# Kernel tuning notes

Measured on AMD Instinct MI355X. Metric: run time of the kernel, lower is better.

Reference implementation:

```python
import jax, jax.numpy as jnp
import numpy as np

T, B, H, W, CIN = 20, 16, 128, 128, 2
CH, OUT = 64, 10
BETA, THR = 0.9, 1.0


def spike(u):
    # Heaviside fire (surrogate grad only matters in bwd module)
    return (u > 0.0).astype(u.dtype)


def setup_inputs() -> dict:
    key = jax.random.key(0)
    k0, k1, k2 = jax.random.split(key, 3)
    x_seq = jax.random.normal(k0, (T, B, H, W, CIN), jnp.float32)
    w_conv = jax.random.normal(k1, (3, 3, CIN, CH), jnp.float32) * (1.0 / np.sqrt(9 * CIN))
    b_conv = jnp.zeros((CH,), jnp.float32)
    w_head = jax.random.normal(k2, (CH, OUT), jnp.float32) * (1.0 / np.sqrt(CH))
    b_head = jnp.zeros((OUT,), jnp.float32)
    return {"x_seq": x_seq, "w_conv": w_conv, "b_conv": b_conv,
            "w_head": w_head, "b_head": b_head}


def reference(x_seq, w_conv, b_conv, w_head, b_head):
    # temporal frame differences: [T-1, B, H, W, CIN]
    flow = x_seq[1:] - x_seq[:-1]
    t, b, h, w, c = flow.shape
    # conv is carry-independent: batch it over (time*batch) in one call
    u = jax.lax.conv_general_dilated(
        flow.reshape(t * b, h, w, c), w_conv,
        window_strides=(1, 1), padding='SAME',
        dimension_numbers=('NHWC', 'HWIO', 'NHWC')) + b_conv
    u = u.reshape(t, b, h, w, CH)  # [T-1, B, H, W, CH]

    def step(V, u_t):
        # LIF: leaky integrate, fire, soft reset
        V = BETA * V + u_t
        s = spike(V - THR)
        V = V - s * THR
        y = jnp.mean(s, axis=(1, 2)) @ w_head + b_head  # [B, OUT]
        return V, (y, jnp.mean(s))

    V0 = jnp.zeros((b, h, w, CH), u.dtype)
    _, (logits_seq, sr_seq) = jax.lax.scan(step, V0, u)
    readout = jnp.mean(logits_seq, axis=0)  # 'mean' readout
    return readout, logits_seq, jnp.asarray([jnp.mean(sr_seq)])
```

## Files before the change

kernel.cpp:

```cpp
#include <hip/hip_runtime.h>
#include <hip/hip_bf16.h>

#define TT   20
#define TS   19
#define BB   16
#define HH   128
#define WW   128
#define CINN 2
#define CHN  64
#define NOUT 10
#define BETA 0.9f
#define INVB (1.0f / BETA)
#define THRV 1.0f

#define NCHUNK 5
#define NPB    128
#define SR_IDX (BB*NOUT + TS*BB*NOUT)

#define LROW  20

typedef __attribute__((ext_vector_type(8))) short short8;
typedef __attribute__((ext_vector_type(4))) float float4v;
typedef __attribute__((ext_vector_type(4))) int   int4v;

__device__ __forceinline__ unsigned rne16(float f) {
    unsigned u = __float_as_uint(f);
    return (u + 0x7fffu + ((u >> 16) & 1u)) >> 16;
}
__device__ __forceinline__ float b2f(unsigned us) { return __uint_as_float(us << 16); }
__device__ __forceinline__ unsigned rndb(float f) {
    unsigned u = __float_as_uint(f);
    return u + 0x7fffu + ((u >> 16) & 1u);
}
__device__ __forceinline__ void pack2(float d0, float d1, unsigned &hi, unsigned &lo) {
    unsigned r0 = rndb(d0), r1 = rndb(d1);
    hi = __builtin_amdgcn_perm(r1, r0, 0x07060302u);
    float e0 = d0 - __uint_as_float(r0 & 0xffff0000u);
    float e1 = d1 - __uint_as_float(r1 & 0xffff0000u);
    lo = __builtin_amdgcn_perm(rndb(e1), rndb(e0), 0x07060302u);
}

__global__ __launch_bounds__(256, 4) void lif_main(const float* __restrict__ x,
                                                   const float* __restrict__ w_conv,
                                                   const float* __restrict__ b_conv,
                                                   int* __restrict__ ws,
                                                   float* __restrict__ out) {
    __shared__ unsigned lds[4][2][2][4 * LROW];
    __shared__ int lds_cnt[NCHUNK][CHN];

    const float2* xp2 = (const float2*)x;
    const int FRAME2  = BB * HH * WW;

    const int tid  = threadIdx.x;
    const int lane = tid & 63;
    const int wv   = __builtin_amdgcn_readfirstlane(tid >> 6);
    const int bx   = blockIdx.x;
    const int r0   = blockIdx.y << 1;
    const int bz   = blockIdx.z;
    const int q    = lane >> 4;
    const int col  = lane & 15;
    const int x0   = (bx << 6) + (wv << 4);
    const int qsh  = q << 3;

    if (bx == 0 && blockIdx.y == 0 && bz == 0) {
        if (tid < BB * NOUT) out[tid] = 0.f;
        else if (tid == BB * NOUT) out[SR_IDX] = 0.f;
    }

    if (tid < NCHUNK * CHN - 256) ((int*)lds_cnt)[256 + tid] = 0;
    ((int*)lds_cnt)[tid] = 0;
    __syncthreads();

    const int  row0 = lane / 18, dx0 = lane - row0 * 18;
    const int  y0s  = r0 - 1 + row0;
    const int  px0s = x0 - 1 + dx0;
    const bool val0 = ((unsigned)y0s < (unsigned)HH) && ((unsigned)px0s < (unsigned)WW);
    const int  off0 = val0 ? (y0s * WW + px0s) : 0;
    const int  ls0  = row0 * LROW + dx0;

    const bool act1 = (lane < 8);
    const int  y1s  = r0 + 2;
    const int  px1s = x0 - 1 + 10 + lane;
    const bool val1 = act1 && ((unsigned)y1s < (unsigned)HH) && ((unsigned)px1s < (unsigned)WW);
    const int  off1 = val1 ? (y1s * WW + px1s) : 0;
    const int  ls1  = 3 * LROW + 10 + lane;

    const int rq  = (q < 3) ? q : 0;
    const int rdb = rq * LROW + col;

    short8 Bh[4], Bl[4];
#pragma unroll
    for (int cg = 0; cg < 4; ++cg) {
        int hi_i[4] = {0, 0, 0, 0}, lo_i[4] = {0, 0, 0, 0};
        if (q < 3) {
#pragma unroll
            for (int j = 0; j < 6; ++j) {
                float w = w_conv[((q * 3 + (j >> 1)) * 2 + (j & 1)) * CHN + cg * 16 + col];
                unsigned hs = rne16(w);
                unsigned ls = rne16(w - b2f(hs));
                hi_i[j >> 1] |= (int)(hs << (16 * (j & 1)));
                lo_i[j >> 1] |= (int)(ls << (16 * (j & 1)));
            }
        }
        int4v hv = {hi_i[0], hi_i[1], hi_i[2], hi_i[3]};
        int4v lv = {lo_i[0], lo_i[1], lo_i[2], lo_i[3]};
        Bh[cg] = __builtin_bit_cast(short8, hv);
        Bl[cg] = __builtin_bit_cast(short8, lv);
    }

    float nb[4];
#pragma unroll
    for (int cg = 0; cg < 4; ++cg) nb[cg] = -b_conv[cg * 16 + col];

    float4v W0[4], W1[4];
#pragma unroll
    for (int cg = 0; cg < 4; ++cg) {
        W0[cg] = (float4v){0.f, 0.f, 0.f, 0.f};
        W1[cg] = (float4v){0.f, 0.f, 0.f, 0.f};
    }

    float ct = 1.0f;
    float S  = 1.0f;
    int pendA = 0, pendB = 0;
    unsigned cur = 0;

    float2 ra_0 = {0.f, 0.f}, rb_0 = {0.f, 0.f}, rc_0 = {0.f, 0.f};
    float2 ra_1 = {0.f, 0.f}, rb_1 = {0.f, 0.f}, rc_1 = {0.f, 0.f};
    const float2* xb = xp2 + bz * HH * WW;
    if (val0) { rb_0 = xb[off0]; ra_0 = xb[FRAME2 + off0]; rc_0 = xb[2 * FRAME2 + off0]; }
    if (val1) { rb_1 = xb[off1]; ra_1 = xb[FRAME2 + off1]; rc_1 = xb[2 * FRAME2 + off1]; }
    {
        unsigned* hiW = &lds[wv][0][0][0];
        unsigned* loW = &lds[wv][0][1][0];
        {
            float d0 = (ra_0.x - rb_0.x), d1 = (ra_0.y - rb_0.y);
            unsigned hw, lw; pack2(d0, d1, hw, lw);
            hiW[ls0] = hw; loW[ls0] = lw;
        }
        if (act1) {
            float d0 = (ra_1.x - rb_1.x), d1 = (ra_1.y - rb_1.y);
            unsigned hw, lw; pack2(d0, d1, hw, lw);
            hiW[ls1] = hw; loW[ls1] = lw;
        }
        rb_0 = ra_0; ra_0 = rc_0;
        rb_1 = ra_1; ra_1 = rc_1;
        if (val0) rc_0 = xb[3 * FRAME2 + off0];
        if (val1) rc_1 = xb[3 * FRAME2 + off1];
    }
    const float2* xn = xb + 4 * FRAME2;

#define STEP(T_, CURB, NXTB, DPOS, DODEF, DOFLUSH, CK, DOSTAGE, DOPREF) do {    \
    const unsigned* hiR = &lds[wv][CURB][0][0] + rdb;                           \
    const unsigned* loR = &lds[wv][CURB][1][0] + rdb;                           \
    unsigned h0 = hiR[0], h1 = hiR[1], h2 = hiR[2];                             \
    unsigned h3 = hiR[LROW], h4 = hiR[LROW + 1], h5 = hiR[LROW + 2];            \
    unsigned l0 = loR[0], l1 = loR[1], l2 = loR[2];                             \
    unsigned l3 = loR[LROW], l4 = loR[LROW + 1], l5 = loR[LROW + 2];            \
    int cp1_ = 0, sh2_ = 0;                                                     \
    if (DODEF) { cp1_ = pendA + pendB; sh2_ = __shfl_xor(cp1_, 32); }           \
    float ctn = ct * INVB;                                                      \
    if (DOSTAGE) {                                                              \
        unsigned* hiW = &lds[wv][NXTB][0][0];                                   \
        unsigned* loW = &lds[wv][NXTB][1][0];                                   \
        {                                                                       \
            float d0 = (ra_0.x - rb_0.x) * ctn;                                 \
            float d1 = (ra_0.y - rb_0.y) * ctn;                                 \
            unsigned hw, lw; pack2(d0, d1, hw, lw);                             \
            hiW[ls0] = hw; loW[ls0] = lw;                                       \
        }                                                                       \
        if (act1) {                                                             \
            float d0 = (ra_1.x - rb_1.x) * ctn;                                 \
            float d1 = (ra_1.y - rb_1.y) * ctn;                                 \
            unsigned hw, lw; pack2(d0, d1, hw, lw);                             \
            hiW[ls1] = hw; loW[ls1] = lw;                                       \
        }                                                                       \
        rb_0 = ra_0; ra_0 = rc_0;                                               \
        rb_1 = ra_1; ra_1 = rc_1;                                               \
        if (DOPREF) {                                                           \
            if (val0) rc_0 = xn[off0];                                          \
            if (val1) rc_1 = xn[off1];                                          \
            xn += FRAME2;                                                       \
        }                                                                       \
    }                                                                           \
    int4v a0h = {(int)h0, (int)h1, (int)h2, (int)h0};                           \
    int4v a0l = {(int)l0, (int)l1, (int)l2, (int)l0};                           \
    int4v a1h = {(int)h3, (int)h4, (int)h5, (int)h3};                           \
    int4v a1l = {(int)l3, (int)l4, (int)l5, (int)l3};                           \
    short8 A0h = __builtin_bit_cast(short8, a0h);                               \
    short8 A0l = __builtin_bit_cast(short8, a0l);                               \
    short8 A1h = __builtin_bit_cast(short8, a1h);                               \
    short8 A1l = __builtin_bit_cast(short8, a1l);                               \
    __builtin_amdgcn_s_setprio(1);                                              \
    _Pragma("unroll")                                                           \
    for (int cg = 0; cg < 4; ++cg) {                                            \
        W0[cg] = __builtin_amdgcn_mfma_f32_16x16x32_bf16(A0h, Bh[cg], W0[cg], 0, 0, 0); \
        W1[cg] = __builtin_amdgcn_mfma_f32_16x16x32_bf16(A1h, Bh[cg], W1[cg], 0, 0, 0); \
    }                                                                           \
    _Pragma("unroll")                                                           \
    for (int cg = 0; cg < 4; ++cg) {                                            \
        W0[cg] = __builtin_amdgcn_mfma_f32_16x16x32_bf16(A0l, Bh[cg], W0[cg], 0, 0, 0); \
        W1[cg] = __builtin_amdgcn_mfma_f32_16x16x32_bf16(A1l, Bh[cg], W1[cg], 0, 0, 0); \
    }                                                                           \
    _Pragma("unroll")                                                           \
    for (int cg = 0; cg < 4; ++cg) {                                            \
        W0[cg] = __builtin_amdgcn_mfma_f32_16x16x32_bf16(A0h, Bl[cg], W0[cg], 0, 0, 0); \
        W1[cg] = __builtin_amdgcn_mfma_f32_16x16x32_bf16(A1h, Bl[cg], W1[cg], 0, 0, 0); \
    }                                                                           \
    __builtin_amdgcn_s_setprio(0);                                              \
    if (DODEF) {                                                                \
        unsigned cnt_ = ((unsigned)(cp1_ + sh2_) >> qsh) & 255u;                \
        cur |= cnt_ << (8 * (DPOS));                                            \
        if (DOFLUSH) { atomicAdd(&lds_cnt[CK][lane], (int)cur); cur = 0u; }     \
    }                                                                           \
    int cpack = 0;                                                              \
    _Pragma("unroll")                                                           \
    for (int cg = 0; cg < 4; ++cg) {                                            \
        float thr = fmaf(nb[cg], S, ct);                                        \
        float4v w0 = W0[cg], w1 = W1[cg];                                       \
        int c = 0;                                                              \
        _Pragma("unroll")                                                       \
        for (int r = 0; r < 4; ++r) {                                           \
            float v0 = w0[r]; bool s0 = v0 > thr;                               \
            w0[r] = s0 ? (v0 - ct) : v0; c += s0;                               \
            float v1 = w1[r]; bool s1 = v1 > thr;                               \
            w1[r] = s1 ? (v1 - ct) : v1; c += s1;                               \
        }                                                                       \
        W0[cg] = w0; W1[cg] = w1;                                               \
        cpack |= c << (8 * cg);                                                 \
    }                                                                           \
    pendA = cpack;                                                              \
    pendB = __shfl_xor(cpack, 16);                                              \
    ct = ctn; S += ctn;                                                         \
} while (0)

#pragma unroll 1
    for (int c = 0; c < 4; ++c) {
        STEP(4 * c + 0, 0, 1, 3, (c > 0), (c > 0), (c - 1), 1, 1);
        STEP(4 * c + 1, 1, 0, 0, 1, 0, 0, 1, 1);
        STEP(4 * c + 2, 0, 1, 1, 1, 0, 0, 1, 1);
        STEP(4 * c + 3, 1, 0, 2, 1, 0, 0, 1, 1);
    }
    STEP(16, 0, 1, 3, 1, 1, 3, 1, 0);
    STEP(17, 1, 0, 0, 1, 0, 0, 1, 0);
    STEP(18, 0, 1, 1, 1, 0, 0, 0, 0);
#undef STEP

    {
        int cp1 = pendA + pendB;
        int cp2 = cp1 + __shfl_xor(cp1, 32);
        unsigned cnt = ((unsigned)cp2 >> qsh) & 255u;
        cur |= cnt << 16;
        atomicAdd(&lds_cnt[4][lane], (int)cur);
    }
    __syncthreads();

    {
        const int pb = (blockIdx.y << 1) | bx;
        const int k0 = tid >> 6, ch = tid & 63;
        ws[((bz * NCHUNK + k0) * NPB + pb) * CHN + ch] = lds_cnt[k0][ch];
        if (tid < CHN)
            ws[((bz * NCHUNK + 4) * NPB + pb) * CHN + tid] = lds_cnt[4][tid];
    }
}

__global__ __launch_bounds__(64) void head_kernel(const int* __restrict__ ws,
                                                  const float* __restrict__ w_head,
                                                  const float* __restrict__ b_head,
                                                  float* __restrict__ out) {
    const int t = blockIdx.x, b = blockIdx.y, ch = threadIdx.x;
    const int k = t >> 2, sh = (t & 3) << 3;
    const int* base = ws + ((b * NCHUNK + k) * NPB) * CHN + ch;

    int cnt = 0;
#pragma unroll 8
    for (int p = 0; p < NPB; ++p) cnt += (base[p * CHN] >> sh) & 255;

    const float s = (float)cnt * (1.f / (HH * WW));
    float acc[NOUT];
#pragma unroll
    for (int o = 0; o < NOUT; ++o) acc[o] = s * w_head[ch * NOUT + o];
    float tt = (float)cnt;
#pragma unroll
    for (int off = 32; off > 0; off >>= 1) {
#pragma unroll
        for (int o = 0; o < NOUT; ++o) acc[o] += __shfl_down(acc[o], off);
        tt += __shfl_down(tt, off);
    }
    if (ch == 0) {
#pragma unroll
        for (int o = 0; o < NOUT; ++o) {
            float lg = acc[o] + b_head[o];
            out[BB * NOUT + (t * BB + b) * NOUT + o] = lg;
            atomicAdd(&out[b * NOUT + o], lg * (1.f / TS));
        }
        atomicAdd(&out[SR_IDX], tt * (1.f / ((float)TS * BB * HH * WW * CHN)));
    }
}

extern "C" void kernel_launch(void* const* d_in, const int* in_sizes, int n_in,
                              void* d_out, int out_size, void* d_ws, size_t ws_size,
                              hipStream_t stream) {
    (void)in_sizes; (void)n_in; (void)ws_size; (void)out_size;
    const float* x      = (const float*)d_in[0];
    const float* w_conv = (const float*)d_in[1];
    const float* b_conv = (const float*)d_in[2];
    const float* w_head = (const float*)d_in[3];
    const float* b_head = (const float*)d_in[4];
    float* out = (float*)d_out;
    int*   ws  = (int*)d_ws;

    lif_main<<<dim3(2, HH / 2, BB), 256, 0, stream>>>(x, w_conv, b_conv, ws, out);
    head_kernel<<<dim3(TS, BB), 64, 0, stream>>>(ws, w_head, b_head, out);
}
```

Baseline: 164.2 us.

## Precompute padded bf16 hi/lo flow frames in workspace before LIF kernel

Adds a flow_pack kernel that computes frame differences, pre-scales them by the leak factor, splits them into bf16 hi/lo pairs and writes them into zero-padded planes in the workspace. The main LIF kernel then loads the MFMA A operands straight from global memory with vector loads, with no LDS staging, halo handling or per-step packing, and double-buffers the next frame's loads. This costs an extra kernel launch and a workspace round trip of roughly the input size. The old path is kept as a fallback when the workspace is too small.

Result: slower. 171.6 us (+4.5%).

```diff
diff --git a/kernel.cpp b/kernel.cpp
--- a/kernel.cpp
+++ b/kernel.cpp
@@ -11,17 +11,29 @@
 #define NOUT 10
 #define BETA 0.9f
 #define INVB (1.0f / BETA)
-#define THRV 1.0f
 
 #define NCHUNK 5
 #define NPB    128
 #define SR_IDX (BB*NOUT + TS*BB*NOUT)
 
+#define PPD      132
+#define ROWB     (PPD*4)
+#define PROWS    129
+#define PLANE_B  (PROWS*ROWB)
+#define FRAME_B  (2*PLANE_B)
+#define FLOW_B   ((size_t)BB*TS*FRAME_B)
+#define SLACK_B  528
+#define CNT_OFF4 ((size_t)(FLOW_B + SLACK_B) / 4)
+#define CNT_B    ((size_t)BB*NCHUNK*NPB*CHN*4)
+#define WS_NEED  (FLOW_B + SLACK_B + CNT_B)
+
 #define LROW  20
 
 typedef __attribute__((ext_vector_type(8))) short short8;
 typedef __attribute__((ext_vector_type(4))) float float4v;
 typedef __attribute__((ext_vector_type(4))) int   int4v;
+typedef unsigned uint4v_t __attribute__((ext_vector_type(4)));
+typedef uint4v_t __attribute__((aligned(4))) uint4vu;
 
 __device__ __forceinline__ unsigned rne16(float f) {
     unsigned u = __float_as_uint(f);
@@ -40,16 +52,55 @@
     lo = __builtin_amdgcn_perm(rndb(e1), rndb(e0), 0x07060302u);
 }
 
-__global__ __launch_bounds__(256, 4) void lif_main(const float* __restrict__ x,
+__global__ __launch_bounds__(256) void flow_pack(const float* __restrict__ x,
+                                                 unsigned* __restrict__ wsf) {
+    const int t = blockIdx.x;
+    const int b = blockIdx.y;
+    const int z = blockIdx.z;
+    const int tid = threadIdx.x;
+
+    float ct = 1.f;
+    for (int i = 0; i < t; ++i) ct *= INVB;
+
+    const float2* x0 = (const float2*)x + ((size_t)t * BB + b) * (HH * WW);
+    const float2* x1 = x0 + (size_t)BB * HH * WW;
+    char* fb = (char*)wsf + ((size_t)b * TS + t) * FRAME_B;
+
+#pragma unroll
+    for (int i = 0; i < 8; ++i) {
+        int p  = i * 256 + tid;
+        int y  = (z << 4) + (p >> 7);
+        int px = p & 127;
+        float2 a = x1[y * WW + px], c = x0[y * WW + px];
+        float d0 = (a.x - c.x) * ct, d1 = (a.y - c.y) * ct;
+        unsigned hw, lw; pack2(d0, d1, hw, lw);
+        unsigned off = (unsigned)(y * PPD + px + 1) * 4u;
+        *(unsigned*)(fb + off) = hw;
+        *(unsigned*)(fb + PLANE_B + off) = lw;
+    }
+    if (tid < 128) {
+        int y  = (z << 4) + (tid >> 3);
+        int c  = tid & 7;
+        int pl = c >> 2;
+        int pp = (c & 3) == 0 ? 0 : 128 + (c & 3);
+        *(unsigned*)(fb + pl * PLANE_B + (y * PPD + pp) * 4) = 0u;
+    }
+    if (z == 0) {
+        for (int d = tid; d < 2 * PPD; d += 256) {
+            int pl = d / PPD, pp = d - pl * PPD;
+            *(unsigned*)(fb + pl * PLANE_B + (128 * PPD + pp) * 4) = 0u;
+        }
+        if (t == 0 && b == 0 && tid < PPD)
+            *((unsigned*)((char*)wsf + FLOW_B) + tid) = 0u;
+    }
+}
+
+__global__ __launch_bounds__(256, 4) void lif_fast(const char* __restrict__ flow,
                                                    const float* __restrict__ w_conv,
                                                    const float* __restrict__ b_conv,
-                                                   int* __restrict__ ws,
+                                                   int* __restrict__ cw,
                                                    float* __restrict__ out) {
-    __shared__ unsigned lds[4][2][2][4 * LROW];
     __shared__ int lds_cnt[NCHUNK][CHN];
-
-    const float2* xp2 = (const float2*)x;
-    const int FRAME2  = BB * HH * WW;
 
     const int tid  = threadIdx.x;
     const int lane = tid & 63;
@@ -66,27 +117,16 @@
         if (tid < BB * NOUT) out[tid] = 0.f;
         else if (tid == BB * NOUT) out[SR_IDX] = 0.f;
     }
-
     if (tid < NCHUNK * CHN - 256) ((int*)lds_cnt)[256 + tid] = 0;
     ((int*)lds_cnt)[tid] = 0;
     __syncthreads();
 
-    const int  row0 = lane / 18, dx0 = lane - row0 * 18;
-    const int  y0s  = r0 - 1 + row0;
-    const int  px0s = x0 - 1 + dx0;
-    const bool val0 = ((unsigned)y0s < (unsigned)HH) && ((unsigned)px0s < (unsigned)WW);
-    const int  off0 = val0 ? (y0s * WW + px0s) : 0;
-    const int  ls0  = row0 * LROW + dx0;
-
-    const bool act1 = (lane < 8);
-    const int  y1s  = r0 + 2;
-    const int  px1s = x0 - 1 + 10 + lane;
-    const bool val1 = act1 && ((unsigned)y1s < (unsigned)HH) && ((unsigned)px1s < (unsigned)WW);
-    const int  off1 = val1 ? (y1s * WW + px1s) : 0;
-    const int  ls1  = 3 * LROW + 10 + lane;
-
     const int rq  = (q < 3) ? q : 0;
-    const int rdb = rq * LROW + col;
+    const int yA0 = r0 - 1 + rq, yA1 = yA0 + 1;
+    const int ym0 = ((unsigned)yA0 < (unsigned)HH) ? yA0 : 128;
+    const int ym1 = ((unsigned)yA1 < (unsigned)HH) ? yA1 : 128;
+    const unsigned offH0 = (unsigned)(ym0 * ROWB + (x0 + col) * 4);
+    const unsigned offH1 = (unsigned)(ym1 * ROWB + (x0 + col) * 4);
 
     short8 Bh[4], Bl[4];
 #pragma unroll
@@ -119,8 +159,185 @@
         W1[cg] = (float4v){0.f, 0.f, 0.f, 0.f};
     }
 
-    float ct = 1.0f;
-    float S  = 1.0f;
+    float ct = 1.0f, S = 1.0f;
+    int pendA = 0, pendB = 0;
+    unsigned cur = 0;
+
+    const char* fp = flow + (size_t)bz * TS * FRAME_B;
+    uint4vu eH0 = *(const uint4vu*)(fp + offH0);
+    uint4vu eH1 = *(const uint4vu*)(fp + offH1);
+    uint4vu eL0 = *(const uint4vu*)(fp + PLANE_B + offH0);
+    uint4vu eL1 = *(const uint4vu*)(fp + PLANE_B + offH1);
+    fp += FRAME_B;
+    uint4vu oH0, oH1, oL0, oL1;
+
+#define STEP(T_, CH0, CH1, CL0, CL1, NH0, NH1, NL0, NL1, DPOS, DODEF, DOFLUSH, CK, DOLOAD) do { \
+    int cp1_ = 0, sh2_ = 0;                                                     \
+    if (DODEF) { cp1_ = pendA + pendB; sh2_ = __shfl_xor(cp1_, 32); }           \
+    if (DOLOAD) {                                                               \
+        NH0 = *(const uint4vu*)(fp + offH0);                                    \
+        NH1 = *(const uint4vu*)(fp + offH1);                                    \
+        NL0 = *(const uint4vu*)(fp + PLANE_B + offH0);                          \
+        NL1 = *(const uint4vu*)(fp + PLANE_B + offH1);                          \
+        fp += FRAME_B;                                                          \
+    }                                                                           \
+    float ctn = ct * INVB;                                                      \
+    short8 A0h = __builtin_bit_cast(short8, CH0);                               \
+    short8 A1h = __builtin_bit_cast(short8, CH1);                               \
+    short8 A0l = __builtin_bit_cast(short8, CL0);                               \
+    short8 A1l = __builtin_bit_cast(short8, CL1);                               \
+    __builtin_amdgcn_s_setprio(1);                                              \
+    _Pragma("unroll")                                                           \
+    for (int cg = 0; cg < 4; ++cg) {                                            \
+        W0[cg] = __builtin_amdgcn_mfma_f32_16x16x32_bf16(A0h, Bh[cg], W0[cg], 0, 0, 0); \
+        W1[cg] = __builtin_amdgcn_mfma_f32_16x16x32_bf16(A1h, Bh[cg], W1[cg], 0, 0, 0); \
+    }                                                                           \
+    _Pragma("unroll")                                                           \
+    for (int cg = 0; cg < 4; ++cg) {                                            \
+        W0[cg] = __builtin_amdgcn_mfma_f32_16x16x32_bf16(A0l, Bh[cg], W0[cg], 0, 0, 0); \
+        W1[cg] = __builtin_amdgcn_mfma_f32_16x16x32_bf16(A1l, Bh[cg], W1[cg], 0, 0, 0); \
+    }                                                                           \
+    _Pragma("unroll")                                                           \
+    for (int cg = 0; cg < 4; ++cg) {                                            \
+        W0[cg] = __builtin_amdgcn_mfma_f32_16x16x32_bf16(A0h, Bl[cg], W0[cg], 0, 0, 0); \
+        W1[cg] = __builtin_amdgcn_mfma_f32_16x16x32_bf16(A1h, Bl[cg], W1[cg], 0, 0, 0); \
+    }                                                                           \
+    __builtin_amdgcn_s_setprio(0);                                              \
+    if (DODEF) {                                                                \
+        unsigned cnt_ = ((unsigned)(cp1_ + sh2_) >> qsh) & 255u;                \
+        cur |= cnt_ << (8 * (DPOS));                                            \
+        if (DOFLUSH) { atomicAdd(&lds_cnt[CK][lane], (int)cur); cur = 0u; }     \
+    }                                                                           \
+    int cpack = 0;                                                              \
+    _Pragma("unroll")                                                           \
+    for (int cg = 0; cg < 4; ++cg) {                                            \
+        float thr = fmaf(nb[cg], S, ct);                                        \
+        float4v w0 = W0[cg], w1 = W1[cg];                                       \
+        int c = 0;                                                              \
+        _Pragma("unroll")                                                       \
+        for (int r = 0; r < 4; ++r) {                                           \
+            float v0 = w0[r]; bool s0 = v0 > thr;                               \
+            w0[r] = s0 ? (v0 - ct) : v0; c += s0;                               \
+            float v1 = w1[r]; bool s1 = v1 > thr;                               \
+            w1[r] = s1 ? (v1 - ct) : v1; c += s1;                               \
+        }                                                                       \
+        W0[cg] = w0; W1[cg] = w1;                                               \
+        cpack |= c << (8 * cg);                                                 \
+    }                                                                           \
+    pendA = cpack;                                                              \
+    pendB = __shfl_xor(cpack, 16);                                              \
+    ct = ctn; S += ctn;                                                         \
+} while (0)
+
+#pragma unroll 1
+    for (int c = 0; c < 4; ++c) {
+        STEP(4 * c + 0, eH0, eH1, eL0, eL1, oH0, oH1, oL0, oL1, 3, (c > 0), (c > 0), (c - 1), 1);
+        STEP(4 * c + 1, oH0, oH1, oL0, oL1, eH0, eH1, eL0, eL1, 0, 1, 0, 0, 1);
+        STEP(4 * c + 2, eH0, eH1, eL0, eL1, oH0, oH1, oL0, oL1, 1, 1, 0, 0, 1);
+        STEP(4 * c + 3, oH0, oH1, oL0, oL1, eH0, eH1, eL0, eL1, 2, 1, 0, 0, 1);
+    }
+    STEP(16, eH0, eH1, eL0, eL1, oH0, oH1, oL0, oL1, 3, 1, 1, 3, 1);
+    STEP(17, oH0, oH1, oL0, oL1, eH0, eH1, eL0, eL1, 0, 1, 0, 0, 1);
+    STEP(18, eH0, eH1, eL0, eL1, oH0, oH1, oL0, oL1, 1, 1, 0, 0, 0);
+#undef STEP
+
+    {
+        int cp1 = pendA + pendB;
+        int cp2 = cp1 + __shfl_xor(cp1, 32);
+        unsigned cnt = ((unsigned)cp2 >> qsh) & 255u;
+        cur |= cnt << 16;
+        atomicAdd(&lds_cnt[4][lane], (int)cur);
+    }
+    __syncthreads();
+
+    {
+        const int pb = (blockIdx.y << 1) | bx;
+        const int k0 = tid >> 6, ch = tid & 63;
+        cw[((bz * NCHUNK + k0) * NPB + pb) * CHN + ch] = lds_cnt[k0][ch];
+        if (tid < CHN)
+            cw[((bz * NCHUNK + 4) * NPB + pb) * CHN + tid] = lds_cnt[4][tid];
+    }
+}
+
+__global__ __launch_bounds__(256, 4) void lif_main(const float* __restrict__ x,
+                                                   const float* __restrict__ w_conv,
+                                                   const float* __restrict__ b_conv,
+                                                   int* __restrict__ ws,
+                                                   float* __restrict__ out) {
+    __shared__ unsigned lds[4][2][2][4 * LROW];
+    __shared__ int lds_cnt[NCHUNK][CHN];
+
+    const float2* xp2 = (const float2*)x;
+    const int FRAME2  = BB * HH * WW;
+
+    const int tid  = threadIdx.x;
+    const int lane = tid & 63;
+    const int wv   = __builtin_amdgcn_readfirstlane(tid >> 6);
+    const int bx   = blockIdx.x;
+    const int r0   = blockIdx.y << 1;
+    const int bz   = blockIdx.z;
+    const int q    = lane >> 4;
+    const int col  = lane & 15;
+    const int x0   = (bx << 6) + (wv << 4);
+    const int qsh  = q << 3;
+
+    if (bx == 0 && blockIdx.y == 0 && bz == 0) {
+        if (tid < BB * NOUT) out[tid] = 0.f;
+        else if (tid == BB * NOUT) out[SR_IDX] = 0.f;
+    }
+    if (tid < NCHUNK * CHN - 256) ((int*)lds_cnt)[256 + tid] = 0;
+    ((int*)lds_cnt)[tid] = 0;
+    __syncthreads();
+
+    const int  row0 = lane / 18, dx0 = lane - row0 * 18;
+    const int  y0s  = r0 - 1 + row0;
+    const int  px0s = x0 - 1 + dx0;
+    const bool val0 = ((unsigned)y0s < (unsigned)HH) && ((unsigned)px0s < (unsigned)WW);
+    const int  off0 = val0 ? (y0s * WW + px0s) : 0;
+    const int  ls0  = row0 * LROW + dx0;
+
+    const bool act1 = (lane < 8);
+    const int  y1s  = r0 + 2;
+    const int  px1s = x0 - 1 + 10 + lane;
+    const bool val1 = act1 && ((unsigned)y1s < (unsigned)HH) && ((unsigned)px1s < (unsigned)WW);
+    const int  off1 = val1 ? (y1s * WW + px1s) : 0;
+    const int  ls1  = 3 * LROW + 10 + lane;
+
+    const int rq  = (q < 3) ? q : 0;
+    const int rdb = rq * LROW + col;
+
+    short8 Bh[4], Bl[4];
+#pragma unroll
+    for (int cg = 0; cg < 4; ++cg) {
+        int hi_i[4] = {0, 0, 0, 0}, lo_i[4] = {0, 0, 0, 0};
+        if (q < 3) {
+#pragma unroll
+            for (int j = 0; j < 6; ++j) {
+                float w = w_conv[((q * 3 + (j >> 1)) * 2 + (j & 1)) * CHN + cg * 16 + col];
+                unsigned hs = rne16(w);
+                unsigned ls = rne16(w - b2f(hs));
+                hi_i[j >> 1] |= (int)(hs << (16 * (j & 1)));
+                lo_i[j >> 1] |= (int)(ls << (16 * (j & 1)));
+            }
+        }
+        int4v hv = {hi_i[0], hi_i[1], hi_i[2], hi_i[3]};
+        int4v lv = {lo_i[0], lo_i[1], lo_i[2], lo_i[3]};
+        Bh[cg] = __builtin_bit_cast(short8, hv);
+        Bl[cg] = __builtin_bit_cast(short8, lv);
+    }
+
+    float nb[4];
+#pragma unroll
+    for (int cg = 0; cg < 4; ++cg) nb[cg] = -b_conv[cg * 16 + col];
+
+    float4v W0[4], W1[4];
+#pragma unroll
+    for (int cg = 0; cg < 4; ++cg) {
+        W0[cg] = (float4v){0.f, 0.f, 0.f, 0.f};
+        W1[cg] = (float4v){0.f, 0.f, 0.f, 0.f};
+    }
+
+    float ct = 1.0f, S = 1.0f;
     int pendA = 0, pendB = 0;
     unsigned cur = 0;
 
@@ -263,13 +480,13 @@
     }
 }
 
-__global__ __launch_bounds__(64) void head_kernel(const int* __restrict__ ws,
+__global__ __launch_bounds__(64) void head_kernel(const int* __restrict__ cw,
                                                   const float* __restrict__ w_head,
                                                   const float* __restrict__ b_head,
                                                   float* __restrict__ out) {
     const int t = blockIdx.x, b = blockIdx.y, ch = threadIdx.x;
     const int k = t >> 2, sh = (t & 3) << 3;
-    const int* base = ws + ((b * NCHUNK + k) * NPB) * CHN + ch;
+    const int* base = cw + ((b * NCHUNK + k) * NPB) * CHN + ch;
 
     int cnt = 0;
 #pragma unroll 8
@@ -300,15 +517,23 @@
 extern "C" void kernel_launch(void* const* d_in, const int* in_sizes, int n_in,
                               void* d_out, int out_size, void* d_ws, size_t ws_size,
                               hipStream_t stream) {
-    (void)in_sizes; (void)n_in; (void)ws_size; (void)out_size;
+    (void)in_sizes; (void)n_in; (void)out_size;
     const float* x      = (const float*)d_in[0];
     const float* w_conv = (const float*)d_in[1];
     const float* b_conv = (const float*)d_in[2];
     const float* w_head = (const float*)d_in[3];
     const float* b_head = (const float*)d_in[4];
     float* out = (float*)d_out;
-    int*   ws  = (int*)d_ws;
-
-    lif_main<<<dim3(2, HH / 2, BB), 256, 0, stream>>>(x, w_conv, b_conv, ws, out);
-    head_kernel<<<dim3(TS, BB), 64, 0, stream>>>(ws, w_head, b_head, out);
-}
+
+    if (ws_size >= WS_NEED) {
+        unsigned* wsf = (unsigned*)d_ws;
+        int* cw = (int*)d_ws + CNT_OFF4;
+        flow_pack<<<dim3(TS, BB, 8), 256, 0, stream>>>(x, wsf);
+        lif_fast<<<dim3(2, HH / 2, BB), 256, 0, stream>>>((const char*)d_ws, w_conv, b_conv, cw, out);
+        head_kernel<<<dim3(TS, BB), 64, 0, stream>>>(cw, w_head, b_head, out);
+    } else {
+        int* cw = (int*)d_ws;
+        lif_main<<<dim3(2, HH / 2, BB), 256, 0, stream>>>(x, w_conv, b_conv, cw, out);
+        head_kernel<<<dim3(TS, BB), 64, 0, stream>>>(cw, w_head, b_head, out);
+    }
+}
```
